# Kernel tuning notes

Measured on AMD Instinct MI355X. Metric: run time of the kernel, lower is better.

## Reference

```python
import jax, jax.numpy as jnp
import numpy as np

B, N, H, V, STEP = 16, 50, 128, 40000, 2

def setup_inputs() -> dict:
    key = jax.random.key(0)
    ks = jax.random.split(key, 24)
    def nrm(i, shape, s=0.08):
        return jax.random.normal(ks[i], shape, jnp.float32) * s
    items = jax.random.randint(ks[0], (B, N), 0, V)
    A = jax.random.uniform(ks[1], (B, N, 2 * N), jnp.float32)
    lengths = jax.random.randint(ks[2], (B,), 1, N + 1)
    mask = (jnp.arange(N)[None, :] < lengths[:, None]).astype(jnp.int32)
    emb = nrm(3, (V, H), 0.1).at[0].set(0.0)  # padding_idx=0 row zeroed
    return dict(
        items=items, A=A, mask=mask, emb=emb,
        w_ih=nrm(4, (3 * H, 2 * H)), w_hh=nrm(5, (3 * H, H)),
        b_ih=nrm(6, (3 * H,)), b_hh=nrm(7, (3 * H,)),
        b_iah=nrm(8, (H,)), b_oah=nrm(9, (H,)),
        W_ein=nrm(10, (H, H)), b_ein=nrm(11, (H,)),
        W_eout=nrm(12, (H, H)), b_eout=nrm(13, (H,)),
        W_one=nrm(14, (H, H)), b_one=nrm(15, (H,)),
        W_two=nrm(16, (H, H)), b_two=nrm(17, (H,)),
        w_three=nrm(18, (H,)),
        W_tr=nrm(19, (H, 2 * H)), b_tr=nrm(20, (H,)),
        W_t=nrm(21, (H, H)),
    )

def gnn_cell(A, hidden, w_ih, w_hh, b_ih, b_hh, b_iah, b_oah, W_ein, b_ein, W_eout, b_eout):
    # A: [B,N,2N], hidden: [B,N,H]
    ein = hidden @ W_ein.T + b_ein
    eout = hidden @ W_eout.T + b_eout
    input_in = jnp.einsum('bnm,bmh->bnh', A[:, :, :N], ein) + b_iah
    input_out = jnp.einsum('bnm,bmh->bnh', A[:, :, N:], eout) + b_oah
    inputs = jnp.concatenate([input_in, input_out], axis=-1)  # [B,N,2H]
    gi = inputs @ w_ih.T + b_ih
    gh = hidden @ w_hh.T + b_hh
    i_r, i_i, i_n = jnp.split(gi, 3, axis=-1)
    h_r, h_i, h_n = jnp.split(gh, 3, axis=-1)
    resetgate = jax.nn.sigmoid(i_r + h_r)
    inputgate = jax.nn.sigmoid(i_i + h_i)
    newgate = jnp.tanh(i_n + resetgate * h_n)
    return newgate + inputgate * (hidden - newgate)

def reference(items, A, mask, emb, w_ih, w_hh, b_ih, b_hh, b_iah, b_oah,
              W_ein, b_ein, W_eout, b_eout, W_one, b_one, W_two, b_two,
              w_three, W_tr, b_tr, W_t):
    hidden = emb[items]  # [B,N,H]
    for _ in range(STEP):
        hidden = gnn_cell(A, hidden, w_ih, w_hh, b_ih, b_hh, b_iah, b_oah,
                          W_ein, b_ein, W_eout, b_eout)
    # compute_scores
    lengths = jnp.sum(mask, axis=1)  # all >= 1 by construction
    ht = hidden[jnp.arange(B), lengths - 1]  # [B,H] last valid item
    q1 = (ht @ W_one.T + b_one)[:, None, :]
    q2 = hidden @ W_two.T + b_two
    mexp = mask[..., None].astype(jnp.float32)  # [B,N,1]
    alpha_logits = jax.nn.sigmoid(q1 + q2) @ w_three[:, None]  # [B,N,1]
    alpha = jax.nn.softmax(jnp.where(mexp == 0, -jnp.inf, alpha_logits), axis=1)
    a = jnp.sum(alpha * hidden * mexp, axis=1)  # [B,H]
    a = jnp.concatenate([a, ht], axis=1) @ W_tr.T + b_tr  # hybrid (nonhybrid=False)
    b_emb = emb[1:]  # [V-1,H]
    qt = (hidden * mexp) @ W_t.T  # [B,N,H]
    beta_logits = jnp.einsum('vh,bnh->bvn', b_emb, qt)
    beta_logits = jnp.where(mask[:, None, :] == 0, -jnp.inf, beta_logits)
    beta = jax.nn.softmax(beta_logits, axis=-1)  # [B,V-1,N]
    target = jnp.einsum('bvn,bnh->bvh', beta, qt * mexp)  # [B,V-1,H]
    # scores = sum((a[:,None,:] + target) * b_emb, -1), split to avoid extra buffer
    scores = jnp.einsum('bvh,vh->bv', target, b_emb) + a @ b_emb.T
    return scores  # [B, V-1]
```

## Files before the change

### kernel.cpp

```cpp
#include <hip/hip_runtime.h>

#define BB 16
#define NN 50
#define HH 128
#define VV 40000
#define VO 39999

typedef unsigned short u16;
typedef unsigned int u32;
typedef __attribute__((ext_vector_type(8))) short short8;
typedef __attribute__((ext_vector_type(4))) float f32x4;

#define OFF_HID    0
#define OFF_HID2   102400
#define OFF_QTBF   307200
#define OFF_LEN    411648
#define OFF_WIHT   411664
#define OFF_WHHT   509968
#define OFF_WEINT  559120
#define OFF_WEOUTT 575504
#define OFF_WTWOT  591888
#define OFF_WTT    608272
#define OFF_WONET  624656
#define OFF_WTRT   641040

__device__ __forceinline__ float sigm(float x){ return 1.0f/(1.0f+__expf(-x)); }
__device__ __forceinline__ float b2f(u16 u){
  union { u32 i; float f; } c; c.i = ((u32)u) << 16; return c.f;
}
__device__ __forceinline__ u16 f2b(float f){
  union { float f; u32 i; } c; c.f = f;
  u32 u = c.i;
  return (u16)((u + 0x7fffu + ((u >> 16) & 1u)) >> 16);
}
__device__ __forceinline__ int frag_idx(int b, int n, int k){
  int tile = n>>4, vlo = n&15, kc = k>>5, quad = (k>>3)&3, j = k&7;
  return (((b*4+tile)*4+kc)<<9) + ((quad<<4)+vlo)*8 + j;
}

__global__ void k_pre(const int* __restrict__ items, const float* __restrict__ emb,
                      const float* __restrict__ w_ih, const float* __restrict__ w_hh,
                      const float* __restrict__ W_ein, const float* __restrict__ W_eout,
                      const float* __restrict__ W_two, const float* __restrict__ W_t,
                      const float* __restrict__ W_one, const float* __restrict__ W_tr,
                      float* __restrict__ ws){
  int idx = blockIdx.x*256 + threadIdx.x;
  if (idx < 102400){
    int r = idx >> 7, h = idx & 127;
    ws[OFF_HID + idx] = emb[items[r]*128 + h];
  } else if (idx < 200704){
    int i = idx-102400; int k=i/384, j=i-k*384;
    ws[OFF_WIHT + i] = w_ih[j*256 + k];
  } else if (idx < 249856){
    int i = idx-200704; int k=i/384, j=i-k*384;
    ws[OFF_WHHT + i] = w_hh[j*128 + k];
  } else if (idx < 266240){
    int i = idx-249856; int k=i>>7, h=i&127;
    ws[OFF_WEINT + i] = W_ein[h*128 + k];
  } else if (idx < 282624){
    int i = idx-266240; int k=i>>7, h=i&127;
    ws[OFF_WEOUTT + i] = W_eout[h*128 + k];
  } else if (idx < 299008){
    int i = idx-282624; int k=i>>7, h=i&127;
    ws[OFF_WTWOT + i] = W_two[h*128 + k];
  } else if (idx < 315392){
    int i = idx-299008; int k=i>>7, h=i&127;
    ws[OFF_WTT + i] = W_t[h*128 + k];
  } else if (idx < 331776){
    int i = idx-315392; int k=i>>7, h=i&127;
    ws[OFF_WONET + i] = W_one[h*128 + k];
  } else if (idx < 364544){
    int i = idx-331776; int k=i>>7, h=i&127;
    ws[OFF_WTRT + i] = W_tr[h*256 + k];
  }
}

__global__ void __launch_bounds__(384) k_step(const float* __restrict__ A,
                       const float* __restrict__ b_ein, const float* __restrict__ b_eout,
                       const float* __restrict__ b_iah, const float* __restrict__ b_oah,
                       const float* __restrict__ b_ih, const float* __restrict__ b_hh,
                       float* __restrict__ ws, int srcOff, int dstOff){
  __shared__ float hall[52][128];
  __shared__ float arow[4][104];
  __shared__ float hAl[4][256];
  __shared__ float sAl[4][2];
  __shared__ float inp[4][256];
  __shared__ float gil[4][384];
  __shared__ float ghl[4][384];
  int t = threadIdx.x;
  int tile = blockIdx.x, b = blockIdx.y;
  int n0 = tile*4;
  const float* hsrc = ws + srcOff + b*6400;
  for (int o=t; o<6656; o+=384) hall[o>>7][o&127] = (o<6400) ? hsrc[o] : 0.0f;
  for (int o=t; o<416; o+=384){
    int r=o/104, c=o-r*104;
    arow[r][c] = (c<100 && n0+r<NN) ? A[(size_t)(b*NN+n0+r)*100 + c] : 0.0f;
  }
  __syncthreads();
  for (int o=t; o<1024; o+=384){
    int r = o>>8, kk = o&255;
    int k = kk & 127;
    const float* ar = &arow[r][(kk>>7)*50];
    float acc = 0.0f;
    #pragma unroll 5
    for (int m=0;m<50;m++) acc += ar[m]*hall[m][k];
    hAl[r][kk] = acc;
  }
  if (t < 8){
    int r = t>>1, half = t&1;
    const float* ar = &arow[r][half*50];
    float s = 0.0f;
    for (int m=0;m<50;m++) s += ar[m];
    sAl[r][half] = s;
  }
  __syncthreads();
  for (int o=t; o<1024; o+=384){
    int r = o>>8, c8 = o&255;
    int in_half = (c8 < 128);
    int c = c8 & 127;
    const float* wT = ws + (in_half ? OFF_WEINT : OFF_WEOUTT);
    const float* hv = &hAl[r][in_half ? 0 : 128];
    float acc = in_half ? (b_iah[c] + sAl[r][0]*b_ein[c])
                        : (b_oah[c] + sAl[r][1]*b_eout[c]);
    for (int k=0;k<128;k+=4){
      float4 h4 = *(const float4*)(hv + k);
      acc += h4.x*wT[(k+0)*128+c] + h4.y*wT[(k+1)*128+c]
           + h4.z*wT[(k+2)*128+c] + h4.w*wT[(k+3)*128+c];
    }
    inp[r][c8] = acc;
  }
  __syncthreads();
  {
    int j = t;
    float gi[4], gh[4];
    float bi2 = b_ih[j], bh2 = b_hh[j];
    #pragma unroll
    for (int r=0;r<4;r++){ gi[r]=bi2; gh[r]=bh2; }
    const float* wti = ws + OFF_WIHT;
    const float* wth = ws + OFF_WHHT;
    for (int k=0;k<256;k+=4){
      float w0 = wti[(k+0)*384+j], w1 = wti[(k+1)*384+j];
      float w2 = wti[(k+2)*384+j], w3_ = wti[(k+3)*384+j];
      #pragma unroll
      for (int r=0;r<4;r++){
        float4 iv = *(const float4*)(&inp[r][k]);
        gi[r] += iv.x*w0 + iv.y*w1 + iv.z*w2 + iv.w*w3_;
      }
    }
    for (int k=0;k<128;k+=4){
      float w0 = wth[(k+0)*384+j], w1 = wth[(k+1)*384+j];
      float w2 = wth[(k+2)*384+j], w3_ = wth[(k+3)*384+j];
      #pragma unroll
      for (int r=0;r<4;r++){
        float4 hv = *(const float4*)(&hall[n0+r][k]);
        gh[r] += hv.x*w0 + hv.y*w1 + hv.z*w2 + hv.w*w3_;
      }
    }
    #pragma unroll
    for (int r=0;r<4;r++){ gil[r][j]=gi[r]; ghl[r][j]=gh[r]; }
  }
  __syncthreads();
  for (int o=t; o<512; o+=384){
    int r=o>>7, h=o&127, row=n0+r;
    if (row<NN){
      float ir_=gil[r][h], ii=gil[r][128+h], inw=gil[r][256+h];
      float hr_=ghl[r][h], hi2=ghl[r][128+h], hn=ghl[r][256+h];
      float rg=sigm(ir_+hr_), ig=sigm(ii+hi2), ng=tanhf(inw+rg*hn);
      float hv=hall[n0+r][h];
      ws[dstOff + (b*NN+row)*128 + h] = ng + ig*(hv-ng);
    }
  }
}

__global__ void __launch_bounds__(512) k_postattn(const int* __restrict__ mask,
                      const float* __restrict__ b_two, const float* __restrict__ b_one,
                      const float* __restrict__ w_three, const float* __restrict__ b_tr,
                      float* __restrict__ ws){
  __shared__ float hid[50][128];
  __shared__ float q2l[50*129];
  __shared__ float htl[128], q1l[128], w3l[128], al[128], pt2[128];
  __shared__ float alg[64];
  __shared__ int lenl;
  int t = threadIdx.x, b = blockIdx.x;
  const float* hsrc = ws + OFF_HID + b*6400;
  for (int o=t;o<6400;o+=512) hid[o>>7][o&127] = hsrc[o];
  if (t==0){
    int len=0;
    for (int n=0;n<NN;n++) len += mask[b*NN+n];
    if (len<1) len=1; if (len>NN) len=NN;
    lenl = len;
    ((int*)(ws+OFF_LEN))[b] = len;
  }
  if (t<128) w3l[t] = w_three[t];
  __syncthreads();
  int len = lenl;
  u16* qtbf = (u16*)(ws + OFF_QTBF);
  for (int o=t; o<12800; o+=512){
    bool isq2 = o < 6400;
    int oo = isq2 ? o : o-6400;
    int n = oo>>7, h = oo&127;
    const float* wT = ws + (isq2 ? OFF_WTWOT : OFF_WTT);
    const float* hv = hid[n];
    float acc = isq2 ? b_two[h] : 0.0f;
    for (int k=0;k<128;k+=4){
      float4 h4 = *(const float4*)(hv + k);
      acc += h4.x*wT[(k+0)*128+h] + h4.y*wT[(k+1)*128+h]
           + h4.z*wT[(k+2)*128+h] + h4.w*wT[(k+3)*128+h];
    }
    if (isq2) q2l[n*129+h] = acc;
    else      qtbf[frag_idx(b, n, h)] = f2b((n<len) ? acc : 0.0f);
  }
  for (int e=t; e<1536; e+=512){
    int kc = e/384, rem2 = e - kc*384;
    int quad = rem2/96, vv = rem2 - quad*96;
    int vlo = 4 + vv/8, j = vv & 7;
    qtbf[(((b*4+3)*4+kc)<<9) + ((quad<<4)+vlo)*8 + j] = 0;
  }
  __syncthreads();
  if (t<128) htl[t] = hid[len-1][t];
  __syncthreads();
  if (t<128){
    const float* w1T = ws + OFF_WONET;
    float q1 = b_one[t];
    for (int k=0;k<128;k+=4){
      float4 h4 = *(const float4*)(htl + k);
      q1 += h4.x*w1T[(k+0)*128+t] + h4.y*w1T[(k+1)*128+t]
          + h4.z*w1T[(k+2)*128+t] + h4.w*w1T[(k+3)*128+t];
    }
    q1l[t] = q1;
  }
  __syncthreads();
  if (t < 200){
    int n = t>>2, part = t&3;
    if (n < len){
      const float* qr  = q2l + n*129 + part*32;
      const float* q1p = q1l + part*32;
      const float* w3p = w3l + part*32;
      float s = 0.0f;
      for (int h=0;h<32;h++) s += w3p[h]*sigm(q1p[h]+qr[h]);
      s += __shfl_xor(s,1); s += __shfl_xor(s,2);
      if (part==0) alg[n] = s;
    }
  }
  __syncthreads();
  if (t < 64){
    float v = (t<len) ? alg[t] : -1e30f;
    float m = v;
    m = fmaxf(m, __shfl_xor(m,1));  m = fmaxf(m, __shfl_xor(m,2));
    m = fmaxf(m, __shfl_xor(m,4));  m = fmaxf(m, __shfl_xor(m,8));
    m = fmaxf(m, __shfl_xor(m,16)); m = fmaxf(m, __shfl_xor(m,32));
    float e = (t<len) ? __expf(v - m) : 0.0f;
    float ss = e;
    ss += __shfl_xor(ss,1);  ss += __shfl_xor(ss,2);
    ss += __shfl_xor(ss,4);  ss += __shfl_xor(ss,8);
    ss += __shfl_xor(ss,16); ss += __shfl_xor(ss,32);
    float inv = 1.0f/ss;
    if (t<len) alg[t] = e*inv;
  }
  __syncthreads();
  if (t < 128){
    float a = 0.0f;
    for (int n=0;n<len;n++) a += alg[n]*hid[n][t];
    al[t] = a;
  }
  __syncthreads();
  float p1 = 0.0f;
  if (t < 256){
    int g2 = t>>7, h = t&127;
    const float* wtr = ws + OFF_WTRT + g2*128*128;
    const float* src = g2 ? htl : al;
    float p = 0.0f;
    for (int k=0;k<128;k++) p += src[k]*wtr[k*128+h];
    if (g2) pt2[h] = p; else p1 = p;
  }
  __syncthreads();
  if (t < 128){
    float af = b_tr[t] + p1 + pt2[t];
    u16 hi = f2b(af);
    u16 lo = f2b(af - b2f(hi));
    qtbf[frag_idx(b, 50, t)] = hi;
    qtbf[frag_idx(b, 51, t)] = lo;
  }
}

__global__ void __launch_bounds__(256) k_scores(const float* __restrict__ emb,
                                                const float* __restrict__ ws,
                                                float* __restrict__ out){
  __shared__ u16 qlds[8192];
  int tid = threadIdx.x;
  int lane = tid & 63, wave = tid >> 6;
  int quad = lane >> 4, vlo = lane & 15;
  int v = blockIdx.y*64 + wave*16 + vlo;
  int vc = (v < VO) ? v : (VO-1);
  const float* erow = emb + (size_t)(vc+1)*128;
  short8 bfr[4];
  #pragma unroll
  for (int kc=0;kc<4;kc++){
    const float4* p = (const float4*)(erow + kc*32 + quad*8);
    float4 x = p[0], y = p[1];
    union { short8 s; u32 w[4]; } u;
    u.w[0] = (u32)f2b(x.x) | ((u32)f2b(x.y)<<16);
    u.w[1] = (u32)f2b(x.z) | ((u32)f2b(x.w)<<16);
    u.w[2] = (u32)f2b(y.x) | ((u32)f2b(y.y)<<16);
    u.w[3] = (u32)f2b(y.z) | ((u32)f2b(y.w)<<16);
    bfr[kc] = u.s;
  }
  const u16* qtf = (const u16*)(ws + OFF_QTBF);
  const int* slen = (const int*)(ws + OFF_LEN);
  int b0 = blockIdx.x*4;
  for (int bi=0;bi<4;bi++){
    int b = b0 + bi;
    __syncthreads();
    {
      const uint4* src = (const uint4*)qtf + (size_t)b*1024;
      uint4* dst = (uint4*)qlds;
      #pragma unroll
      for (int r=0;r<4;r++) dst[tid + r*256] = src[tid + r*256];
    }
    __syncthreads();
    int len = slen[b];
    f32x4 acc0={0.f,0.f,0.f,0.f}, acc1=acc0, acc2=acc0, acc3=acc0;
    #pragma unroll
    for (int kc=0;kc<4;kc++){
      const u16* base = qlds + kc*512 + lane*8;
      short8 a0 = *(const short8*)(base + 0*2048);
      short8 a1 = *(const short8*)(base + 1*2048);
      short8 a2 = *(const short8*)(base + 2*2048);
      short8 a3 = *(const short8*)(base + 3*2048);
      acc0 = __builtin_amdgcn_mfma_f32_16x16x32_bf16(a0, bfr[kc], acc0, 0,0,0);
      acc1 = __builtin_amdgcn_mfma_f32_16x16x32_bf16(a1, bfr[kc], acc1, 0,0,0);
      acc2 = __builtin_amdgcn_mfma_f32_16x16x32_bf16(a2, bfr[kc], acc2, 0,0,0);
      acc3 = __builtin_amdgcn_mfma_f32_16x16x32_bf16(a3, bfr[kc], acc3, 0,0,0);
    }
    int nb = quad*4;
    float ss=0.f, nm=0.f;
    #pragma unroll
    for (int r=0;r<4;r++){
      { int n=nb+r;    if(n<len){ float e=__expf(acc0[r]); ss+=e; nm+=e*acc0[r]; } }
      { int n=nb+r+16; if(n<len){ float e=__expf(acc1[r]); ss+=e; nm+=e*acc1[r]; } }
      { int n=nb+r+32; if(n<len){ float e=__expf(acc2[r]); ss+=e; nm+=e*acc2[r]; } }
      { int n=nb+r+48; if(n<len){ float e=__expf(acc3[r]); ss+=e; nm+=e*acc3[r]; } }
    }
    ss += __shfl_xor(ss,16); ss += __shfl_xor(ss,32);
    nm += __shfl_xor(nm,16); nm += __shfl_xor(nm,32);
    if (quad==0 && v < VO){
      float pa = acc3[2] + acc3[3];
      out[(size_t)b*VO + v] = nm/ss + pa;
    }
  }
}

extern "C" void kernel_launch(void* const* d_in, const int* in_sizes, int n_in,
                              void* d_out, int out_size, void* d_ws, size_t ws_size,
                              hipStream_t stream){
  const int*   items  = (const int*)d_in[0];
  const float* A      = (const float*)d_in[1];
  const int*   mask   = (const int*)d_in[2];
  const float* emb    = (const float*)d_in[3];
  const float* w_ih   = (const float*)d_in[4];
  const float* w_hh   = (const float*)d_in[5];
  const float* b_ih   = (const float*)d_in[6];
  const float* b_hh   = (const float*)d_in[7];
  const float* b_iah  = (const float*)d_in[8];
  const float* b_oah  = (const float*)d_in[9];
  const float* W_ein  = (const float*)d_in[10];
  const float* b_ein  = (const float*)d_in[11];
  const float* W_eout = (const float*)d_in[12];
  const float* b_eout = (const float*)d_in[13];
  const float* W_one  = (const float*)d_in[14];
  const float* b_one  = (const float*)d_in[15];
  const float* W_two  = (const float*)d_in[16];
  const float* b_two  = (const float*)d_in[17];
  const float* w_three= (const float*)d_in[18];
  const float* W_tr   = (const float*)d_in[19];
  const float* b_tr   = (const float*)d_in[20];
  const float* W_t    = (const float*)d_in[21];
  float* ws  = (float*)d_ws;
  float* out = (float*)d_out;

  k_pre<<<1424,256,0,stream>>>(items,emb,w_ih,w_hh,W_ein,W_eout,W_two,W_t,W_one,W_tr,ws);
  k_step<<<dim3(13,16),384,0,stream>>>(A,b_ein,b_eout,b_iah,b_oah,b_ih,b_hh,ws,OFF_HID,OFF_HID2);
  k_step<<<dim3(13,16),384,0,stream>>>(A,b_ein,b_eout,b_iah,b_oah,b_ih,b_hh,ws,OFF_HID2,OFF_HID);
  k_postattn<<<16,512,0,stream>>>(mask,b_two,b_one,w_three,b_tr,ws);
  k_scores<<<dim3(4,625),256,0,stream>>>(emb,ws,out);
}
```

Measured before the change: 252.5 us.

## Split post-attention kernel into wide projection kernel and small attention kernel

The 16-block post-attention kernel is split in two. A 264-block kernel computes the q2 and qt projections over 8-row tiles with register blocking, zeroes the padding fragments, and computes ht and q1. A second 16-block kernel then does the softmax attention and the hybrid projection. This spreads the projection work across many more compute units at the cost of one extra launch and a round trip through global memory for q2, q1 and ht.

```diff
diff --git a/kernel.cpp b/kernel.cpp
--- a/kernel.cpp
+++ b/kernel.cpp
@@ -13,6 +13,9 @@
 
 #define OFF_HID    0
 #define OFF_HID2   102400
+#define OFF_Q2     102400
+#define OFF_Q1     204800
+#define OFF_HT     206848
 #define OFF_QTBF   307200
 #define OFF_LEN    411648
 #define OFF_WIHT   411664
@@ -172,63 +175,93 @@
   }
 }
 
-__global__ void __launch_bounds__(512) k_postattn(const int* __restrict__ mask,
+__global__ void __launch_bounds__(256) k_post(const int* __restrict__ mask,
                       const float* __restrict__ b_two, const float* __restrict__ b_one,
-                      const float* __restrict__ w_three, const float* __restrict__ b_tr,
                       float* __restrict__ ws){
-  __shared__ float hid[50][128];
-  __shared__ float q2l[50*129];
-  __shared__ float htl[128], q1l[128], w3l[128], al[128], pt2[128];
-  __shared__ float alg[64];
-  __shared__ int lenl;
-  int t = threadIdx.x, b = blockIdx.x;
-  const float* hsrc = ws + OFF_HID + b*6400;
-  for (int o=t;o<6400;o+=512) hid[o>>7][o&127] = hsrc[o];
-  if (t==0){
-    int len=0;
-    for (int n=0;n<NN;n++) len += mask[b*NN+n];
-    if (len<1) len=1; if (len>NN) len=NN;
-    lenl = len;
-    ((int*)(ws+OFF_LEN))[b] = len;
-  }
-  if (t<128) w3l[t] = w_three[t];
-  __syncthreads();
-  int len = lenl;
+  int bx = blockIdx.x, t = threadIdx.x;
   u16* qtbf = (u16*)(ws + OFF_QTBF);
-  for (int o=t; o<12800; o+=512){
-    bool isq2 = o < 6400;
-    int oo = isq2 ? o : o-6400;
-    int n = oo>>7, h = oo&127;
+  if (bx < 200){
+    bool isq2 = bx < 100;
+    int r0 = (isq2 ? bx : bx-100) * 8;
+    __shared__ float hl[1024];
+    for (int i=0;i<4;i++) hl[t+i*256] = ws[OFF_HID + r0*128 + t + i*256];
+    __syncthreads();
+    int h = t & 127, g = t >> 7;
     const float* wT = ws + (isq2 ? OFF_WTWOT : OFF_WTT);
-    const float* hv = hid[n];
-    float acc = isq2 ? b_two[h] : 0.0f;
-    for (int k=0;k<128;k+=4){
-      float4 h4 = *(const float4*)(hv + k);
-      acc += h4.x*wT[(k+0)*128+h] + h4.y*wT[(k+1)*128+h]
-           + h4.z*wT[(k+2)*128+h] + h4.w*wT[(k+3)*128+h];
-    }
-    if (isq2) q2l[n*129+h] = acc;
-    else      qtbf[frag_idx(b, n, h)] = f2b((n<len) ? acc : 0.0f);
-  }
-  for (int e=t; e<1536; e+=512){
-    int kc = e/384, rem2 = e - kc*384;
-    int quad = rem2/96, vv = rem2 - quad*96;
-    int vlo = 4 + vv/8, j = vv & 7;
-    qtbf[(((b*4+3)*4+kc)<<9) + ((quad<<4)+vlo)*8 + j] = 0;
-  }
-  __syncthreads();
-  if (t<128) htl[t] = hid[len-1][t];
-  __syncthreads();
-  if (t<128){
-    const float* w1T = ws + OFF_WONET;
-    float q1 = b_one[t];
-    for (int k=0;k<128;k+=4){
-      float4 h4 = *(const float4*)(htl + k);
-      q1 += h4.x*w1T[(k+0)*128+t] + h4.y*w1T[(k+1)*128+t]
-          + h4.z*w1T[(k+2)*128+t] + h4.w*w1T[(k+3)*128+t];
-    }
-    q1l[t] = q1;
-  }
+    float binit = isq2 ? b_two[h] : 0.0f;
+    float acc[4];
+    #pragma unroll
+    for (int r=0;r<4;r++) acc[r] = binit;
+    for (int k4=0;k4<32;k4++){
+      int k = k4*4;
+      float w0 = wT[(k+0)*128+h], w1 = wT[(k+1)*128+h];
+      float w2 = wT[(k+2)*128+h], w3 = wT[(k+3)*128+h];
+      #pragma unroll
+      for (int r=0;r<4;r++){
+        float4 hv = *(const float4*)(hl + (g*4+r)*128 + k);
+        acc[r] += hv.x*w0 + hv.y*w1 + hv.z*w2 + hv.w*w3;
+      }
+    }
+    #pragma unroll
+    for (int r=0;r<4;r++){
+      int row = r0 + g*4 + r;
+      if (isq2) ws[OFF_Q2 + row*128 + h] = acc[r];
+      else {
+        float val = mask[row] ? acc[r] : 0.0f;
+        int b = row/NN, n = row - b*NN;
+        qtbf[frag_idx(b, n, h)] = f2b(val);
+      }
+    }
+  } else if (bx < 248){
+    int i = (bx-200)*256 + t;
+    #pragma unroll
+    for (int kk=0;kk<2;kk++){
+      int e = i*2 + kk;
+      int b = e/1536, rem = e - b*1536;
+      int kc = rem/384, rem2 = rem - kc*384;
+      int quad = rem2/96, vv = rem2 - quad*96;
+      int vlo = 4 + vv/8, j = vv & 7;
+      qtbf[(((b*4+3)*4+kc)<<9) + ((quad<<4)+vlo)*8 + j] = 0;
+    }
+  } else {
+    __shared__ float htl[128];
+    int b = bx - 248;
+    if (t < 128){
+      int len = 0;
+      for (int n=0;n<NN;n++) len += mask[b*NN+n];
+      if (len<1) len=1; if (len>NN) len=NN;
+      float ht = ws[OFF_HID + (b*NN + len-1)*128 + t];
+      ws[OFF_HT + b*128 + t] = ht;
+      htl[t] = ht;
+      if (t==0) ((int*)(ws+OFF_LEN))[b] = len;
+    }
+    __syncthreads();
+    if (t < 128){
+      const float* w1T = ws + OFF_WONET;
+      float q1 = b_one[t];
+      for (int k=0;k<128;k+=4){
+        float4 h4 = *(const float4*)(htl + k);
+        q1 += h4.x*w1T[(k+0)*128+t] + h4.y*w1T[(k+1)*128+t]
+            + h4.z*w1T[(k+2)*128+t] + h4.w*w1T[(k+3)*128+t];
+      }
+      ws[OFF_Q1 + b*128 + t] = q1;
+    }
+  }
+}
+
+__global__ void __launch_bounds__(256) k_attn2(const float* __restrict__ w_three,
+                        const float* __restrict__ b_tr, float* __restrict__ ws){
+  __shared__ float q2l[NN*129];
+  __shared__ float q1l[128], w3l[128], htl[128], al[128], pt2[128], alg[64];
+  int t = threadIdx.x;
+  int b = blockIdx.x;
+  for (int o=t;o<6400;o+=256){ int n=o>>7, h=o&127; q2l[n*129+h] = ws[OFF_Q2 + b*6400 + o]; }
+  if (t < 128){
+    q1l[t] = ws[OFF_Q1 + b*128 + t];
+    w3l[t] = w_three[t];
+    htl[t] = ws[OFF_HT + b*128 + t];
+  }
+  int len = ((const int*)(ws+OFF_LEN))[b];
   __syncthreads();
   if (t < 200){
     int n = t>>2, part = t&3;
@@ -259,8 +292,9 @@
   }
   __syncthreads();
   if (t < 128){
+    const float* hid = ws + OFF_HID + b*6400;
     float a = 0.0f;
-    for (int n=0;n<len;n++) a += alg[n]*hid[n][t];
+    for (int n=0;n<len;n++) a += alg[n]*hid[n*128+t];
     al[t] = a;
   }
   __syncthreads();
@@ -278,6 +312,7 @@
     float af = b_tr[t] + p1 + pt2[t];
     u16 hi = f2b(af);
     u16 lo = f2b(af - b2f(hi));
+    u16* qtbf = (u16*)(ws + OFF_QTBF);
     qtbf[frag_idx(b, 50, t)] = hi;
     qtbf[frag_idx(b, 51, t)] = lo;
   }
@@ -381,6 +416,7 @@
   k_pre<<<1424,256,0,stream>>>(items,emb,w_ih,w_hh,W_ein,W_eout,W_two,W_t,W_one,W_tr,ws);
   k_step<<<dim3(13,16),384,0,stream>>>(A,b_ein,b_eout,b_iah,b_oah,b_ih,b_hh,ws,OFF_HID,OFF_HID2);
   k_step<<<dim3(13,16),384,0,stream>>>(A,b_ein,b_eout,b_iah,b_oah,b_ih,b_hh,ws,OFF_HID2,OFF_HID);
-  k_postattn<<<16,512,0,stream>>>(mask,b_two,b_one,w_three,b_tr,ws);
+  k_post<<<264,256,0,stream>>>(mask,b_two,b_one,ws);
+  k_attn2<<<16,256,0,stream>>>(w_three,b_tr,ws);
   k_scores<<<dim3(4,625),256,0,stream>>>(emb,ws,out);
 }
```

New measurement: 213.9 us. -15.3%, faster.
